# Optimization experiments

Measured on AMD Instinct MI355X. Metric: run time of the kernel, lower is better.

## Reference

```python
import jax, jax.numpy as jnp
import numpy as np

N_NODES = 50000
N_EDGES = 800000
IN_FEATS = 256
OUT_FEATS = 64


def setup_inputs() -> dict:
    key = jax.random.key(0)
    k1, k2, k3, k4 = jax.random.split(key, 4)
    feat = jax.random.normal(k1, (N_NODES, IN_FEATS), dtype=jnp.float32)
    src = jax.random.randint(k2, (N_EDGES,), 0, N_NODES, dtype=jnp.int32)
    dst = jax.random.randint(k3, (N_EDGES,), 0, N_NODES, dtype=jnp.int32)
    # Glorot-uniform like DGL's GraphConv weight init
    limit = float(np.sqrt(6.0 / (IN_FEATS + OUT_FEATS)))
    W = jax.random.uniform(k4, (IN_FEATS, OUT_FEATS), dtype=jnp.float32,
                           minval=-limit, maxval=limit)
    b = jnp.zeros((OUT_FEATS,), dtype=jnp.float32)
    return {"feat": feat, "src": src, "dst": dst, "W": W, "b": b}


def reference(feat, src, dst, W, b):
    n = feat.shape[0]
    ones = jnp.ones_like(src, dtype=feat.dtype)
    out_deg = jax.ops.segment_sum(ones, src, num_segments=n)
    in_deg = jax.ops.segment_sum(ones, dst, num_segments=n)
    # norm='both': deg^{-1/2}, degrees clamped to min 1 (allow_zero_in_degree)
    norm_src = jax.lax.rsqrt(jnp.maximum(out_deg, 1.0))   # [N]
    norm_dst = jax.lax.rsqrt(jnp.maximum(in_deg, 1.0))    # [N]
    # in_feats > out_feats -> apply weight before aggregation (DGL fast path)
    h = (feat * norm_src[:, None]) @ W                    # [N, out]
    agg = jax.ops.segment_sum(h[src], dst, num_segments=n)  # SpMM: sum messages at dst
    rst = agg * norm_dst[:, None] + b
    return jax.nn.sigmoid(rst)
```

## Files before the change

kernel.cpp:

```cpp
#include <hip/hip_runtime.h>
#include <hip/hip_bf16.h>
#include <math.h>

#define N_NODES 50000
#define N_EDGES 800000
#define IN_F 256
#define OUT_F 64

#define BKT 256
#define NB 196
#define CAP 6144
#define PARTA_BLOCKS 400
#define EPB (N_EDGES / PARTA_BLOCKS)
#define GEMM_BM 32
#define GEMM_BLOCKS 782
#define HIST_CHUNK 12500
#define HIST_BLOCKS 64

typedef __attribute__((ext_vector_type(8))) short bf16x8;
typedef __attribute__((ext_vector_type(4))) float f32x4;

__device__ __forceinline__ ushort f2bf(float x) {
    __hip_bfloat16 b = __float2bfloat16(x);
    return *reinterpret_cast<ushort*>(&b);
}
__device__ __forceinline__ float bf_lo(uint v) { return __uint_as_float(v << 16); }
__device__ __forceinline__ float bf_hi(uint v) { return __uint_as_float(v & 0xffff0000u); }

__global__ __launch_bounds__(256) void prep_kernel(int* __restrict__ bcntD,
                                                   const float* __restrict__ W,
                                                   ushort* __restrict__ Wpk,
                                                   int4* __restrict__ outdeg4) {
    const int tid = threadIdx.x;
    if (blockIdx.x == 0) {
        for (int i = tid; i < NB; i += 256) bcntD[i] = 0;
    } else if (blockIdx.x < 9) {
        const int gid = (blockIdx.x - 1) * 256 + tid;
        const int lane = gid & 63;
        const int ct = (gid >> 6) & 3;
        const int step = gid >> 8;
        const int kg = lane >> 4;
        const int n = lane & 15;
        const float* base = W + (size_t)(step * 32 + kg * 8) * OUT_F + ct * 16 + n;
        union { ushort u[8]; uint4 v; } pk;
        #pragma unroll
        for (int j = 0; j < 8; ++j) pk.u[j] = f2bf(base[(size_t)j * OUT_F]);
        ((uint4*)Wpk)[gid] = pk.v;
    } else {
        const int i = (blockIdx.x - 9) * 256 + tid;
        if (i < N_NODES / 4) outdeg4[i] = (int4){0, 0, 0, 0};
    }
}

__global__ __launch_bounds__(512) void fused_kernel(const int* __restrict__ src,
                                                    const int* __restrict__ dst,
                                                    int* __restrict__ bcntD,
                                                    uint* __restrict__ pairsD,
                                                    int* __restrict__ outdeg,
                                                    const float* __restrict__ feat,
                                                    const ushort* __restrict__ Wpk,
                                                    ushort* __restrict__ h) {
    __shared__ __align__(16) char smem[65536];
    const int bi = blockIdx.x;
    const int tid = threadIdx.x;

    if (bi < 2 * PARTA_BLOCKS && (bi & 1)) {
        int2* ed    = (int2*)smem;
        uint* stgD  = (uint*)(smem + 16000);
        int* lcntD  = (int*)(smem + 24000);
        int* ldofD  = (int*)(smem + 25024);
        int* lbaseD = (int*)(smem + 26048);
        int* wtotD  = (int*)(smem + 26832);
        const int id = bi >> 1;
        const int n4 = EPB / 4;

        for (int i = tid; i < 256; i += 512) lcntD[i] = 0;
        __syncthreads();

        const int4* t4 = (const int4*)(dst + (size_t)id * EPB);
        const int4* s4 = (const int4*)(src + (size_t)id * EPB);
        for (int i = tid; i < n4; i += 512) {
            const int4 d = t4[i];
            const int4 s = s4[i];
            ed[4 * i + 0] = (int2){d.x, s.x};
            ed[4 * i + 1] = (int2){d.y, s.y};
            ed[4 * i + 2] = (int2){d.z, s.z};
            ed[4 * i + 3] = (int2){d.w, s.w};
            atomicAdd(&lcntD[d.x >> 8], 1);
            atomicAdd(&lcntD[d.y >> 8], 1);
            atomicAdd(&lcntD[d.z >> 8], 1);
            atomicAdd(&lcntD[d.w >> 8], 1);
        }
        __syncthreads();

        for (int i = tid; i < NB; i += 512) {
            const int cD = lcntD[i];
            lbaseD[i] = cD ? atomicAdd(&bcntD[i], cD) : 0;
        }

        if (tid < 256) {
            const int lane = tid & 63;
            const int wave = tid >> 6;
            const int vD = lcntD[tid];
            int iD = vD;
            #pragma unroll
            for (int d = 1; d < 64; d <<= 1) {
                const int uD = __shfl_up(iD, d, 64);
                if (lane >= d) iD += uD;
            }
            if (lane == 63) wtotD[wave] = iD;
            ldofD[tid] = iD - vD;
        }
        __syncthreads();
        if (tid < 256) {
            const int wave = tid >> 6;
            int woD = 0;
            #pragma unroll
            for (int w = 0; w < 4; ++w)
                if (w < wave) woD += wtotD[w];
            ldofD[tid] += woD;
            lcntD[tid] = 0;
        }
        __syncthreads();

        for (int i = tid; i < EPB; i += 512) {
            const int2 e = ed[i];
            const int bx = e.x >> 8;
            const int pos = atomicAdd(&lcntD[bx], 1);
            stgD[ldofD[bx] + pos] =
                ((uint)bx << 24) | ((uint)(e.x & 255) << 16) | (uint)e.y;
        }
        __syncthreads();

        for (int i = tid; i < EPB; i += 512) {
            const uint pv = stgD[i];
            const int bD = (int)(pv >> 24);
            pairsD[(size_t)bD * CAP + lbaseD[bD] + (i - ldofD[bD])] = pv & 0xFFFFFFu;
        }
    } else if (bi >= 2 * PARTA_BLOCKS && bi < 2 * PARTA_BLOCKS + 2 * HIST_BLOCKS
               && (bi & 1)) {
        int* cnt = (int*)smem;
        const int id = (bi - 2 * PARTA_BLOCKS) >> 1;
        const int chunk = id >> 4;
        const int slice = id & 15;
        const int base = chunk * HIST_CHUNK;

        for (int i = tid; i < HIST_CHUNK; i += 512) cnt[i] = 0;
        __syncthreads();

        const int4* s4 = (const int4*)(src + (size_t)slice * (N_EDGES / 16));
        for (int i = tid; i < (N_EDGES / 16) / 4; i += 512) {
            const int4 v = s4[i];
            int r;
            r = v.x - base; if ((unsigned)r < (unsigned)HIST_CHUNK) atomicAdd(&cnt[r], 1);
            r = v.y - base; if ((unsigned)r < (unsigned)HIST_CHUNK) atomicAdd(&cnt[r], 1);
            r = v.z - base; if ((unsigned)r < (unsigned)HIST_CHUNK) atomicAdd(&cnt[r], 1);
            r = v.w - base; if ((unsigned)r < (unsigned)HIST_CHUNK) atomicAdd(&cnt[r], 1);
        }
        __syncthreads();

        for (int i = tid; i < HIST_CHUNK; i += 512) {
            const int c = cnt[i];
            if (c) atomicAdd(&outdeg[base + i], c);
        }
    } else {
        const int id = (bi < 2 * PARTA_BLOCKS) ? (bi >> 1)
                     : (bi < 2 * PARTA_BLOCKS + 2 * HIST_BLOCKS)
                         ? (PARTA_BLOCKS + ((bi - 2 * PARTA_BLOCKS) >> 1))
                         : (bi - PARTA_BLOCKS - HIST_BLOCKS);
        const int half = tid >> 8;
        const int t = tid & 255;
        const int lane = t & 63;
        const int wave = t >> 6;
        const int m = lane & 15;
        const int g = lane >> 4;
        const int rowBase = (id * 2 + half) * GEMM_BM;
        float* ftile = (float*)(smem + (size_t)half * 32768);
        const char* fb = (const char*)feat;

        #pragma unroll
        for (int it = 0; it < 8; ++it) {
            const int R = it * 4 + wave;
            const int off = (lane * 16) ^ ((R & 7) << 4);
            int grow = rowBase + R;
            if (grow >= N_NODES) grow = N_NODES - 1;
            __builtin_amdgcn_global_load_lds(
                (const __attribute__((address_space(1))) void*)(fb + ((size_t)grow << 10) + off),
                (__attribute__((address_space(3))) void*)((char*)ftile + it * 4096 + wave * 1024),
                16, 0, 0);
        }
        __syncthreads();

        const int rowHalf = wave & 1;
        const int colHalf = wave >> 1;

        f32x4 acc[2];
        acc[0] = (f32x4){0.f, 0.f, 0.f, 0.f};
        acc[1] = (f32x4){0.f, 0.f, 0.f, 0.f};

        const int Rr = rowHalf * 16 + m;
        const int swz = (Rr & 7) << 4;
        const char* rowb = (const char*)ftile + (Rr << 10);
        const bf16x8* wp = (const bf16x8*)Wpk;

        #pragma unroll
        for (int step = 0; step < 8; ++step) {
            const int kb = step * 128 + g * 32;
            const float4 a0 = *(const float4*)(rowb + (kb ^ swz));
            const float4 a1 = *(const float4*)(rowb + ((kb + 16) ^ swz));
            bf16x8 aa;
            aa[0] = (short)f2bf(a0.x); aa[1] = (short)f2bf(a0.y);
            aa[2] = (short)f2bf(a0.z); aa[3] = (short)f2bf(a0.w);
            aa[4] = (short)f2bf(a1.x); aa[5] = (short)f2bf(a1.y);
            aa[6] = (short)f2bf(a1.z); aa[7] = (short)f2bf(a1.w);
            #pragma unroll
            for (int ct = 0; ct < 2; ++ct)
                acc[ct] = __builtin_amdgcn_mfma_f32_16x16x32_bf16(
                    aa, wp[(step * 4 + colHalf * 2 + ct) * 64 + lane], acc[ct], 0, 0, 0);
        }

        #pragma unroll
        for (int j = 0; j < 4; ++j) {
            const int row = rowBase + rowHalf * 16 + g * 4 + j;
            if (row < N_NODES) {
                #pragma unroll
                for (int ct = 0; ct < 2; ++ct)
                    h[(size_t)row * OUT_F + colHalf * 32 + ct * 16 + m] = f2bf(acc[ct][j]);
            }
        }
    }
}

__global__ __launch_bounds__(1024) void bucket_kernel(const int* __restrict__ outdeg,
                                                      float* __restrict__ normS,
                                                      const uint* __restrict__ pairsD,
                                                      const int* __restrict__ bcntD,
                                                      uint* __restrict__ ptrdeg,
                                                      ushort* __restrict__ sorted_src) {
    __shared__ int cnt[BKT];
    __shared__ int loff[BKT];
    __shared__ int wtot[4];
    const int bb = blockIdx.x;
    const int tid = threadIdx.x;
    const int node = bb * BKT + tid;

    if (tid < BKT) {
        cnt[tid] = 0;
        if (node < N_NODES)
            normS[node] = rsqrtf(fmaxf((float)outdeg[node], 1.0f));
    }
    __syncthreads();
    const int nD = bcntD[bb];
    const uint* pb = pairsD + (size_t)bb * CAP;
    for (int i = tid; i < nD; i += 1024) atomicAdd(&cnt[(pb[i] >> 16) & 255u], 1);
    __syncthreads();

    if (tid < BKT) {
        const int lane = tid & 63;
        const int wave = tid >> 6;
        const int v = cnt[tid];
        int incl = v;
        #pragma unroll
        for (int d = 1; d < 64; d <<= 1) {
            int u = __shfl_up(incl, d, 64);
            if (lane >= d) incl += u;
        }
        if (lane == 63) wtot[wave] = incl;
        loff[tid] = incl - v;
    }
    __syncthreads();
    if (tid < BKT) {
        const int wave = tid >> 6;
        int woff = 0;
        #pragma unroll
        for (int w = 0; w < 4; ++w)
            if (w < wave) woff += wtot[w];
        const int ex = woff + loff[tid];
        loff[tid] = ex;
        const int v = cnt[tid];
        cnt[tid] = 0;
        if (node < N_NODES)
            ptrdeg[node] = (uint)(bb * CAP + ex) | ((uint)v << 21);
    }
    __syncthreads();

    for (int i = tid; i < nD; i += 1024) {
        const uint p = pb[i];
        const int local = (int)((p >> 16) & 255u);
        const int pos = atomicAdd(&cnt[local], 1);
        sorted_src[(size_t)bb * CAP + loff[local] + pos] = (ushort)(p & 0xFFFFu);
    }
}

__global__ __launch_bounds__(256) void gather_kernel(const uint* __restrict__ ptrdeg,
                                                     const ushort* __restrict__ sorted_src,
                                                     const float* __restrict__ normS,
                                                     const ushort* __restrict__ h,
                                                     const float* __restrict__ b,
                                                     float* __restrict__ out) {
    const int lane = threadIdx.x & 63;
    const int q = lane & 15;
    const int g = lane >> 4;
    int nid = (int)((blockIdx.x * (size_t)blockDim.x + threadIdx.x) >> 6);
    if (nid >= N_NODES) return;
    nid = __builtin_amdgcn_readfirstlane(nid);

    const uint pd = ptrdeg[nid];
    const int beg = (int)(pd & 0x1FFFFFu);
    const int deg = (int)(pd >> 21);

    float a0 = 0.f, a1 = 0.f, a2 = 0.f, a3 = 0.f;
    const int nfull = deg >> 2;
    int e = beg + g;
    #pragma unroll 4
    for (int i = 0; i < nfull; ++i) {
        const int s = (int)sorted_src[e];
        e += 4;
        const float ns = normS[s];
        const uint2 v = *(const uint2*)(h + (size_t)s * OUT_F + q * 4);
        a0 = fmaf(ns, bf_lo(v.x), a0); a1 = fmaf(ns, bf_hi(v.x), a1);
        a2 = fmaf(ns, bf_lo(v.y), a2); a3 = fmaf(ns, bf_hi(v.y), a3);
    }
    const int rem = deg & 3;
    if (g < rem) {
        const int s = (int)sorted_src[beg + (deg & ~3) + g];
        const float ns = normS[s];
        const uint2 v = *(const uint2*)(h + (size_t)s * OUT_F + q * 4);
        a0 = fmaf(ns, bf_lo(v.x), a0); a1 = fmaf(ns, bf_hi(v.x), a1);
        a2 = fmaf(ns, bf_lo(v.y), a2); a3 = fmaf(ns, bf_hi(v.y), a3);
    }
    a0 += __shfl_xor(a0, 16, 64); a1 += __shfl_xor(a1, 16, 64);
    a2 += __shfl_xor(a2, 16, 64); a3 += __shfl_xor(a3, 16, 64);
    a0 += __shfl_xor(a0, 32, 64); a1 += __shfl_xor(a1, 32, 64);
    a2 += __shfl_xor(a2, 32, 64); a3 += __shfl_xor(a3, 32, 64);

    if (g == 0) {
        const float norm = rsqrtf(fmaxf((float)deg, 1.0f));
        const float4 bb = *(const float4*)(b + q * 4);
        float4 o;
        o.x = 1.0f / (1.0f + expf(-(a0 * norm + bb.x)));
        o.y = 1.0f / (1.0f + expf(-(a1 * norm + bb.y)));
        o.z = 1.0f / (1.0f + expf(-(a2 * norm + bb.z)));
        o.w = 1.0f / (1.0f + expf(-(a3 * norm + bb.w)));
        *(float4*)(out + (size_t)nid * OUT_F + q * 4) = o;
    }
}

extern "C" void kernel_launch(void* const* d_in, const int* in_sizes, int n_in,
                              void* d_out, int out_size, void* d_ws, size_t ws_size,
                              hipStream_t stream) {
    const float* feat = (const float*)d_in[0];
    const int* src    = (const int*)d_in[1];
    const int* dst    = (const int*)d_in[2];
    const float* W    = (const float*)d_in[3];
    const float* b    = (const float*)d_in[4];
    float* out = (float*)d_out;

    char* ws = (char*)d_ws;
    size_t off = 0;
    ushort* h = (ushort*)(ws + off);        off += (size_t)N_NODES * OUT_F * 2;
    float* normS = (float*)(ws + off);      off += (size_t)N_NODES * 4;
    uint* ptrdeg = (uint*)(ws + off);       off += (size_t)N_NODES * 4;
    int* outdeg = (int*)(ws + off);         off += (size_t)N_NODES * 4;
    int* bcntD = (int*)(ws + off);          off += (size_t)NB * 4 + 16;
    ushort* Wpk = (ushort*)(ws + off);      off += (size_t)IN_F * OUT_F * 2;
    uint* pairsD = (uint*)(ws + off);       off += (size_t)NB * CAP * 4;
    ushort* sorted_src = (ushort*)(ws + off); off += (size_t)NB * CAP * 2;

    prep_kernel<<<9 + (N_NODES / 4 + 255) / 256, 256, 0, stream>>>(
        bcntD, W, Wpk, (int4*)outdeg);

    fused_kernel<<<PARTA_BLOCKS + HIST_BLOCKS + GEMM_BLOCKS, 512, 0, stream>>>(
        src, dst, bcntD, pairsD, outdeg, feat, Wpk, h);

    bucket_kernel<<<NB, 1024, 0, stream>>>(outdeg, normS,
                                           pairsD, bcntD, ptrdeg, sorted_src);

    gather_kernel<<<(N_NODES * 64 + 255) / 256, 256, 0, stream>>>(
        ptrdeg, sorted_src, normS, h, b, out);
}
```

Baseline: 68.03 us.

## Halve fused-kernel shared memory by giving each GEMM block one 32-row tile

Measured after the change: 69.78 us. 1.03x slower.

```diff
diff --git a/kernel.cpp b/kernel.cpp
--- a/kernel.cpp
+++ b/kernel.cpp
@@ -13,9 +13,9 @@
 #define PARTA_BLOCKS 400
 #define EPB (N_EDGES / PARTA_BLOCKS)
 #define GEMM_BM 32
-#define GEMM_BLOCKS 782
-#define HIST_CHUNK 12500
-#define HIST_BLOCKS 64
+#define GEMM_TILES 1563
+#define HIST_CHUNK 8192
+#define HIST_BLOCKS 112
 
 typedef __attribute__((ext_vector_type(8))) short bf16x8;
 typedef __attribute__((ext_vector_type(4))) float f32x4;
@@ -60,7 +60,7 @@
                                                     const float* __restrict__ feat,
                                                     const ushort* __restrict__ Wpk,
                                                     ushort* __restrict__ h) {
-    __shared__ __align__(16) char smem[65536];
+    __shared__ __align__(16) char smem[33664];
     const int bi = blockIdx.x;
     const int tid = threadIdx.x;
 
@@ -161,42 +161,38 @@
 
         for (int i = tid; i < HIST_CHUNK; i += 512) {
             const int c = cnt[i];
-            if (c) atomicAdd(&outdeg[base + i], c);
+            if (c && base + i < N_NODES) atomicAdd(&outdeg[base + i], c);
         }
     } else {
         const int id = (bi < 2 * PARTA_BLOCKS) ? (bi >> 1)
                      : (bi < 2 * PARTA_BLOCKS + 2 * HIST_BLOCKS)
                          ? (PARTA_BLOCKS + ((bi - 2 * PARTA_BLOCKS) >> 1))
                          : (bi - PARTA_BLOCKS - HIST_BLOCKS);
-        const int half = tid >> 8;
-        const int t = tid & 255;
-        const int lane = t & 63;
-        const int wave = t >> 6;
+        const int lane = tid & 63;
+        const int wave = tid >> 6;
         const int m = lane & 15;
         const int g = lane >> 4;
-        const int rowBase = (id * 2 + half) * GEMM_BM;
-        float* ftile = (float*)(smem + (size_t)half * 32768);
+        const int rowBase = id * GEMM_BM;
+        float* ftile = (float*)smem;
         const char* fb = (const char*)feat;
 
         #pragma unroll
-        for (int it = 0; it < 8; ++it) {
-            const int R = it * 4 + wave;
+        for (int it = 0; it < 4; ++it) {
+            const int R = it * 8 + wave;
             const int off = (lane * 16) ^ ((R & 7) << 4);
             int grow = rowBase + R;
             if (grow >= N_NODES) grow = N_NODES - 1;
             __builtin_amdgcn_global_load_lds(
                 (const __attribute__((address_space(1))) void*)(fb + ((size_t)grow << 10) + off),
-                (__attribute__((address_space(3))) void*)((char*)ftile + it * 4096 + wave * 1024),
+                (__attribute__((address_space(3))) void*)((char*)ftile + it * 8192 + wave * 1024),
                 16, 0, 0);
         }
         __syncthreads();
 
         const int rowHalf = wave & 1;
-        const int colHalf = wave >> 1;
-
-        f32x4 acc[2];
-        acc[0] = (f32x4){0.f, 0.f, 0.f, 0.f};
-        acc[1] = (f32x4){0.f, 0.f, 0.f, 0.f};
+        const int ct = wave >> 1;
+
+        f32x4 acc = (f32x4){0.f, 0.f, 0.f, 0.f};
 
         const int Rr = rowHalf * 16 + m;
         const int swz = (Rr & 7) << 4;
@@ -213,20 +209,15 @@
             aa[2] = (short)f2bf(a0.z); aa[3] = (short)f2bf(a0.w);
             aa[4] = (short)f2bf(a1.x); aa[5] = (short)f2bf(a1.y);
             aa[6] = (short)f2bf(a1.z); aa[7] = (short)f2bf(a1.w);
-            #pragma unroll
-            for (int ct = 0; ct < 2; ++ct)
-                acc[ct] = __builtin_amdgcn_mfma_f32_16x16x32_bf16(
-                    aa, wp[(step * 4 + colHalf * 2 + ct) * 64 + lane], acc[ct], 0, 0, 0);
+            acc = __builtin_amdgcn_mfma_f32_16x16x32_bf16(
+                aa, wp[(step * 4 + ct) * 64 + lane], acc, 0, 0, 0);
         }
 
         #pragma unroll
         for (int j = 0; j < 4; ++j) {
             const int row = rowBase + rowHalf * 16 + g * 4 + j;
-            if (row < N_NODES) {
-                #pragma unroll
-                for (int ct = 0; ct < 2; ++ct)
-                    h[(size_t)row * OUT_F + colHalf * 32 + ct * 16 + m] = f2bf(acc[ct][j]);
-            }
+            if (row < N_NODES)
+                h[(size_t)row * OUT_F + ct * 16 + m] = f2bf(acc[j]);
         }
     }
 }
@@ -370,7 +361,9 @@
     prep_kernel<<<9 + (N_NODES / 4 + 255) / 256, 256, 0, stream>>>(
         bcntD, W, Wpk, (int4*)outdeg);
 
-    fused_kernel<<<PARTA_BLOCKS + HIST_BLOCKS + GEMM_BLOCKS, 512, 0, stream>>>(
+    fused_kernel<<<2 * PARTA_BLOCKS + 2 * HIST_BLOCKS +
+                       (GEMM_TILES - PARTA_BLOCKS - HIST_BLOCKS),
+                   512, 0, stream>>>(
         src, dst, bcntD, pairsD, outdeg, feat, Wpk, h);
 
     bucket_kernel<<<NB, 1024, 0, stream>>>(outdeg, normS,
```
